# Kernel optimization log

Measured on AMD Instinct MI355X. Metric: run time of the kernel, lower is better.

The kernel has to match this reference:

```python
import jax, jax.numpy as jnp
import numpy as np

LORA_ALPHA = 16.0

def setup_inputs() -> dict:
    key = jax.random.key(0)
    kx, kw, ka, kb, kbias = jax.random.split(key, 5)
    B_, S, D_in, D_out, R = 2, 4096, 4096, 4096, 16
    x = jax.random.normal(kx, (B_, S, D_in), dtype=jnp.float32)
    W = jax.random.normal(kw, (D_out, D_in), dtype=jnp.float32) * 0.02
    A = jax.random.normal(ka, (R, D_in), dtype=jnp.float32) * 0.02
    Bm = jax.random.normal(kb, (D_out, R), dtype=jnp.float32) * 0.02
    bias = jax.random.normal(kbias, (D_out,), dtype=jnp.float32) * 0.02
    return {"x": x, "W": W, "A": A, "B": Bm, "bias": bias}

def reference(x, W, A, B, bias):
    # y = x @ W.T + bias + (alpha/rank) * (x @ A.T) @ B.T   (dropout p=0)
    rank = A.shape[0]
    lora_scale = LORA_ALPHA / rank
    y = jnp.einsum('bsd,nd->bsn', x, W) + bias
    h = jnp.einsum('bsd,rd->bsr', x, A)          # [B,S,r] low-rank down-proj
    y = y + lora_scale * jnp.einsum('bsr,nr->bsn', h, B)
    return y
```

## Files before the change

### kernel.cpp

```cpp
#include <hip/hip_runtime.h>
#include <hip/hip_bf16.h>

typedef short bf16x8 __attribute__((ext_vector_type(8)));
typedef float f32x4 __attribute__((ext_vector_type(4)));
typedef unsigned short ushort8v __attribute__((ext_vector_type(8)));

#define SBAR() asm volatile("s_barrier" ::: "memory")
#define LGKM0() do { asm volatile("s_waitcnt lgkmcnt(0)" ::: "memory"); \
    __builtin_amdgcn_sched_barrier(0); } while (0)

__device__ __forceinline__ unsigned short f2bf(float f) {
  unsigned u = __builtin_bit_cast(unsigned, f);
  u += 0x7fffu + ((u >> 16) & 1u);
  return (unsigned short)(u >> 16);
}

__device__ __forceinline__ void gload_lds16(const unsigned short* g, unsigned short* l) {
  __builtin_amdgcn_global_load_lds((const __attribute__((address_space(1))) void*)g,
                                   (__attribute__((address_space(3))) void*)l, 16, 0, 0);
}

__global__ __launch_bounds__(256) void prep_kernel(const float* __restrict__ x,
                                                   const float* __restrict__ W,
                                                   const float* __restrict__ A,
                                                   const float* __restrict__ Bm,
                                                   unsigned short* __restrict__ xb,
                                                   unsigned short* __restrict__ wb,
                                                   float scale, int K, int R, int n8, int t8) {
  int i = blockIdx.x * 256 + threadIdx.x;
  if (i < n8) {
    const float4* p = (const float4*)x + (size_t)i * 2;
    float4 a = p[0], b = p[1];
    ushort8v v;
    v[0] = f2bf(a.x); v[1] = f2bf(a.y); v[2] = f2bf(a.z); v[3] = f2bf(a.w);
    v[4] = f2bf(b.x); v[5] = f2bf(b.y); v[6] = f2bf(b.z); v[7] = f2bf(b.w);
    *((ushort8v*)xb + i) = v;
    return;
  }
  int idx = i - n8;
  if (idx >= t8) return;
  int perRow = K >> 3;
  int n = idx / perRow;
  int d0 = (idx - n * perRow) << 3;
  const float4* wp = (const float4*)(W + (size_t)n * K + d0);
  float4 w0 = wp[0], w1 = wp[1];
  float acc[8] = {w0.x, w0.y, w0.z, w0.w, w1.x, w1.y, w1.z, w1.w};
#pragma unroll 4
  for (int r = 0; r < R; ++r) {
    float c = Bm[(size_t)n * R + r] * scale;
    const float4* ap = (const float4*)(A + (size_t)r * K + d0);
    float4 a0 = ap[0], a1 = ap[1];
    acc[0] += c * a0.x; acc[1] += c * a0.y; acc[2] += c * a0.z; acc[3] += c * a0.w;
    acc[4] += c * a1.x; acc[5] += c * a1.y; acc[6] += c * a1.z; acc[7] += c * a1.w;
  }
  ushort8v v;
#pragma unroll
  for (int j = 0; j < 8; ++j) v[j] = f2bf(acc[j]);
  *((ushort8v*)wb + idx) = v;
}

__global__ __launch_bounds__(512, 2) void gemm256_bt_bias(const unsigned short* __restrict__ Xb,
                                                          const unsigned short* __restrict__ Wb,
                                                          const float* __restrict__ bias,
                                                          float* __restrict__ C,
                                                          int M, int N, int K) {
  __shared__ __align__(16) char lds[131072];
  const int t = threadIdx.x;
  const int wave = t >> 6, lane = t & 63;
  const int fr = lane & 15, kc = lane >> 4;
  const int wr = wave >> 2, wc = wave & 3;

  const int NTn = N >> 8;
  const int nwg = gridDim.x;
  int bid = blockIdx.x;
  if ((nwg & 7) == 0) bid = (bid & 7) * (nwg >> 3) + (bid >> 3);
  const int tm = bid / NTn, tn = bid % NTn;
  const int m0 = tm << 8, n0 = tn << 8;

  const int grow = t >> 3;
  const int gch8 = ((t & 7) ^ ((t >> 3) & 7)) << 3;
  const size_t K64 = (size_t)64 * K;
  const unsigned short* pa = Xb + (size_t)(m0 + grow) * K + gch8;
  const unsigned short* pb = Wb + (size_t)(n0 + grow) * K + gch8;
  char* const sb = (char*)lds + wave * 1024;

  const int sw  = (lane & 7) << 4;
  const int cb0 = (kc << 4) ^ sw;
  const int cb1 = cb0 ^ 64;
  const int rowA = (wr * 128 + fr) * 128;
  const int rowB = 32768 + (wc * 64 + fr) * 128;
  const char* rA0[2] = { (char*)lds + rowA + cb0, (char*)lds + 65536 + rowA + cb0 };
  const char* rA1[2] = { (char*)lds + rowA + cb1, (char*)lds + 65536 + rowA + cb1 };
  const char* rB0[2] = { (char*)lds + rowB + cb0, (char*)lds + 65536 + rowB + cb0 };
  const char* rB1[2] = { (char*)lds + rowB + cb1, (char*)lds + 65536 + rowB + cb1 };

  f32x4 acc[8][4];
#pragma unroll
  for (int m = 0; m < 8; ++m)
#pragma unroll
    for (int n = 0; n < 4; ++n) acc[m][n] = (f32x4){0.f, 0.f, 0.f, 0.f};

  bf16x8 aQa[8], aQb[8], bQ0[4], bQ1[4];
  const int NT = K >> 6;

#define STG_A1(BUF, s) gload_lds16(pa + (size_t)(s) * K64, \
    (unsigned short*)(sb + ((BUF) ? 65536 : 0) + (s) * 8192))
#define STG_B1(BUF, s) gload_lds16(pb + (size_t)(s) * K64, \
    (unsigned short*)(sb + ((BUF) ? 65536 : 0) + 32768 + (s) * 8192))

#define MM(qm, qn, AR, BR) do { \
    __builtin_amdgcn_s_setprio(1); \
    _Pragma("unroll") for (int ks = 0; ks < 2; ++ks) \
    _Pragma("unroll") for (int m = 0; m < 4; ++m) \
    _Pragma("unroll") for (int n = 0; n < 2; ++n) \
      acc[(qm)*4+m][(qn)*2+n] = __builtin_amdgcn_mfma_f32_16x16x32_bf16( \
          AR[m*2+ks], BR[n*2+ks], acc[(qm)*4+m][(qn)*2+n], 0, 0, 0); \
    __builtin_amdgcn_s_setprio(0); } while (0)

#define STEP(BUF, DOSTG, VM2, VM4) do { \
     \
    aQa[0]=*(const bf16x8*)(rA0[BUF]);        aQa[1]=*(const bf16x8*)(rA1[BUF]); \
    aQa[2]=*(const bf16x8*)(rA0[BUF]+2048);   aQa[3]=*(const bf16x8*)(rA1[BUF]+2048); \
    aQa[4]=*(const bf16x8*)(rA0[BUF]+4096);   aQa[5]=*(const bf16x8*)(rA1[BUF]+4096); \
    aQa[6]=*(const bf16x8*)(rA0[BUF]+6144);   aQa[7]=*(const bf16x8*)(rA1[BUF]+6144); \
    bQ0[0]=*(const bf16x8*)(rB0[BUF]);        bQ0[1]=*(const bf16x8*)(rB1[BUF]); \
    bQ0[2]=*(const bf16x8*)(rB0[BUF]+2048);   bQ0[3]=*(const bf16x8*)(rB1[BUF]+2048); \
    if (DOSTG) { STG_B1(BUF^1, 0); STG_B1(BUF^1, 1); } \
    asm volatile("s_waitcnt lgkmcnt(8)" ::: "memory"); \
    SBAR(); LGKM0(); MM(0, 0, aQa, bQ0); SBAR(); \
     \
    bQ1[0]=*(const bf16x8*)(rB0[BUF]+4096);   bQ1[1]=*(const bf16x8*)(rB1[BUF]+4096); \
    bQ1[2]=*(const bf16x8*)(rB0[BUF]+6144);   bQ1[3]=*(const bf16x8*)(rB1[BUF]+6144); \
    if (DOSTG) { STG_B1(BUF^1, 2); STG_B1(BUF^1, 3); } \
    asm volatile("s_waitcnt vmcnt(" VM2 ")" ::: "memory"); \
    SBAR(); LGKM0(); MM(0, 1, aQa, bQ1); SBAR(); \
     \
    aQb[0]=*(const bf16x8*)(rA0[BUF]+8192);   aQb[1]=*(const bf16x8*)(rA1[BUF]+8192); \
    aQb[2]=*(const bf16x8*)(rA0[BUF]+10240);  aQb[3]=*(const bf16x8*)(rA1[BUF]+10240); \
    aQb[4]=*(const bf16x8*)(rA0[BUF]+12288);  aQb[5]=*(const bf16x8*)(rA1[BUF]+12288); \
    aQb[6]=*(const bf16x8*)(rA0[BUF]+14336);  aQb[7]=*(const bf16x8*)(rA1[BUF]+14336); \
    if (DOSTG) { STG_A1(BUF^1, 0); STG_A1(BUF^1, 2); } \
    SBAR(); LGKM0(); MM(1, 0, aQb, bQ0); SBAR(); \
     \
    if (DOSTG) { STG_A1(BUF^1, 1); STG_A1(BUF^1, 3); pa += 64; pb += 64; } \
    asm volatile("s_waitcnt vmcnt(" VM4 ")" ::: "memory"); \
    SBAR(); MM(1, 1, aQb, bQ1); SBAR(); \
  } while (0)

  STG_B1(0, 0); STG_B1(0, 1); STG_B1(0, 2); STG_B1(0, 3);
  STG_A1(0, 0); STG_A1(0, 2); STG_A1(0, 1); STG_A1(0, 3);
  pa += 64; pb += 64;
  asm volatile("s_waitcnt vmcnt(2)" ::: "memory");
  SBAR();

  for (int cc = 0; cc < NT - 2; cc += 2) {
    STEP(0, 1, "4", "2");
    STEP(1, 1, "4", "2");
  }
  STEP(0, 1, "4", "2");
  STEP(1, 0, "0", "0");

  const int crow = (lane >> 4) * 4;
  const int ccol = lane & 15;
#pragma unroll
  for (int n = 0; n < 4; ++n) {
    int col = n0 + wc * 64 + n * 16 + ccol;
    float bv = bias[col];
#pragma unroll
    for (int m = 0; m < 8; ++m) {
      int row = m0 + wr * 128 + m * 16 + crow;
      float* cp = C + (size_t)row * N + col;
#pragma unroll
      for (int r = 0; r < 4; ++r) cp[(size_t)r * N] = acc[m][n][r] + bv;
    }
  }
#undef STG_A1
#undef STG_B1
#undef MM
#undef STEP
}

__global__ __launch_bounds__(256) void gemm_bt_bias(const unsigned short* __restrict__ Xb,
                                                    const unsigned short* __restrict__ Wb,
                                                    const float* __restrict__ bias,
                                                    float* __restrict__ C,
                                                    int M, int N, int K) {
  __shared__ unsigned short sA[128 * 32];
  __shared__ unsigned short sB[128 * 32];
  const int t = threadIdx.x;
  const int wave = t >> 6, lane = t & 63;
  const int NT = N >> 7;
  const int nwg = gridDim.x;
  int bid = blockIdx.x;
  if ((nwg & 7) == 0) bid = (bid & 7) * (nwg >> 3) + (bid >> 3);
  const int tm = bid / NT, tn = bid % NT;
  const int m0 = tm << 7, n0 = tn << 7;
  const int wr = wave >> 1, wc = wave & 1;

  f32x4 acc[4][4];
#pragma unroll
  for (int m = 0; m < 4; ++m)
#pragma unroll
    for (int n = 0; n < 4; ++n) acc[m][n] = (f32x4){0.f, 0.f, 0.f, 0.f};

  const unsigned short* gA0 = Xb + (size_t)(m0 + (t >> 2)) * K + (t & 3) * 8;
  const unsigned short* gA1 = Xb + (size_t)(m0 + 64 + (t >> 2)) * K + (t & 3) * 8;
  const unsigned short* gB0 = Wb + (size_t)(n0 + (t >> 2)) * K + (t & 3) * 8;
  const unsigned short* gB1 = Wb + (size_t)(n0 + 64 + (t >> 2)) * K + (t & 3) * 8;
  unsigned short* lA0 = sA + (size_t)(wave * 64) * 8;
  unsigned short* lA1 = sA + (size_t)(256 + wave * 64) * 8;
  unsigned short* lB0 = sB + (size_t)(wave * 64) * 8;
  unsigned short* lB1 = sB + (size_t)(256 + wave * 64) * 8;

  const int rrow = lane & 15;
  const int rk = (lane >> 4) * 8;

  for (int k0 = 0; k0 < K; k0 += 32) {
    gload_lds16(gA0 + k0, lA0);
    gload_lds16(gA1 + k0, lA1);
    gload_lds16(gB0 + k0, lB0);
    gload_lds16(gB1 + k0, lB1);
    __syncthreads();
    bf16x8 af[4], bfr[4];
#pragma unroll
    for (int m = 0; m < 4; ++m)
      af[m] = *(const bf16x8*)&sA[(size_t)(wr * 64 + m * 16 + rrow) * 32 + rk];
#pragma unroll
    for (int n = 0; n < 4; ++n)
      bfr[n] = *(const bf16x8*)&sB[(size_t)(wc * 64 + n * 16 + rrow) * 32 + rk];
#pragma unroll
    for (int m = 0; m < 4; ++m)
#pragma unroll
      for (int n = 0; n < 4; ++n)
        acc[m][n] = __builtin_amdgcn_mfma_f32_16x16x32_bf16(af[m], bfr[n], acc[m][n], 0, 0, 0);
    __syncthreads();
  }
  const int crow0 = (lane >> 4) * 4;
  const int ccol = lane & 15;
#pragma unroll
  for (int n = 0; n < 4; ++n) {
    int col = n0 + wc * 64 + n * 16 + ccol;
    float bv = bias[col];
#pragma unroll
    for (int m = 0; m < 4; ++m) {
      int row = m0 + wr * 64 + m * 16 + crow0;
      float* cp = C + (size_t)row * N + col;
#pragma unroll
      for (int r = 0; r < 4; ++r) cp[(size_t)r * N] = acc[m][n][r] + bv;
    }
  }
}

__global__ __launch_bounds__(64) void lora_h_kernel(const float* __restrict__ x,
                                                    const float* __restrict__ A,
                                                    float* __restrict__ h,
                                                    float scale, int K, int R) {
  int m = blockIdx.x, lane = threadIdx.x;
  float acc[16];
#pragma unroll
  for (int r = 0; r < 16; ++r) acc[r] = 0.f;
  for (int d = lane; d < K; d += 64) {
    float xv = x[(size_t)m * K + d];
    for (int r = 0; r < R; ++r) acc[r] += xv * A[(size_t)r * K + d];
  }
  for (int off = 32; off; off >>= 1)
    for (int r = 0; r < R; ++r) acc[r] += __shfl_down(acc[r], off);
  if (lane == 0)
    for (int r = 0; r < R; ++r) h[(size_t)m * R + r] = acc[r] * scale;
}

__global__ __launch_bounds__(256) void fgemm_fallback(const float* __restrict__ X,
                                                      const float* __restrict__ W,
                                                      const float* __restrict__ Bm,
                                                      const float* __restrict__ bias,
                                                      const float* __restrict__ h,
                                                      float* __restrict__ C,
                                                      int M, int N, int K, int R) {
  __shared__ float sX[64][20];
  __shared__ float sW[64][20];
  int nt = N >> 6;
  int bx = blockIdx.x % nt, by = blockIdx.x / nt;
  int m0 = by << 6, n0 = bx << 6;
  int t = threadIdx.x;
  int tx = t & 15, ty = t >> 4;
  float acc[4][4] = {};
  int lr = t >> 2, lc = (t & 3) << 2;
  for (int k0 = 0; k0 < K; k0 += 16) {
    *(float4*)&sX[lr][lc] = *(const float4*)&X[(size_t)(m0 + lr) * K + k0 + lc];
    *(float4*)&sW[lr][lc] = *(const float4*)&W[(size_t)(n0 + lr) * K + k0 + lc];
    __syncthreads();
#pragma unroll
    for (int kk = 0; kk < 16; ++kk) {
      float a[4], b[4];
#pragma unroll
      for (int i = 0; i < 4; ++i) a[i] = sX[ty * 4 + i][kk];
#pragma unroll
      for (int j = 0; j < 4; ++j) b[j] = sW[tx * 4 + j][kk];
#pragma unroll
      for (int i = 0; i < 4; ++i)
#pragma unroll
        for (int j = 0; j < 4; ++j) acc[i][j] += a[i] * b[j];
    }
    __syncthreads();
  }
#pragma unroll
  for (int i = 0; i < 4; ++i) {
    int row = m0 + ty * 4 + i;
#pragma unroll
    for (int j = 0; j < 4; ++j) {
      int col = n0 + tx * 4 + j;
      float lo = 0.f;
      for (int r = 0; r < R; ++r) lo += h[(size_t)row * R + r] * Bm[(size_t)col * R + r];
      C[(size_t)row * N + col] = acc[i][j] + bias[col] + lo;
    }
  }
}

extern "C" void kernel_launch(void* const* d_in, const int* in_sizes, int n_in,
                              void* d_out, int out_size, void* d_ws, size_t ws_size,
                              hipStream_t stream) {
  const float* x    = (const float*)d_in[0];
  const float* W    = (const float*)d_in[1];
  const float* A    = (const float*)d_in[2];
  const float* Bm   = (const float*)d_in[3];
  const float* bias = (const float*)d_in[4];
  float* out = (float*)d_out;

  const int N = in_sizes[4];
  const int R = in_sizes[3] / N;
  const int K = in_sizes[2] / R;
  const int M = in_sizes[0] / K;
  const float scale = 16.0f / (float)R;

  const size_t xbytes = (size_t)M * K * 2;
  const size_t wbytes = (size_t)N * K * 2;
  const bool ws_ok = (ws_size >= xbytes + wbytes);
  const bool fast256 = ws_ok && (M % 256 == 0) && (N % 256 == 0) && (K % 128 == 0) && (K >= 256);
  const bool fast128 = ws_ok && (M % 128 == 0) && (N % 128 == 0) && (K % 32 == 0);

  if (fast256 || fast128) {
    unsigned short* xb = (unsigned short*)d_ws;
    unsigned short* wb = (unsigned short*)((char*)d_ws + xbytes);
    int n8 = M * K / 8;
    int t8 = N * K / 8;
    int total = n8 + t8;
    prep_kernel<<<dim3((total + 255) / 256), dim3(256), 0, stream>>>(x, W, A, Bm, xb, wb,
                                                                     scale, K, R, n8, t8);
    if (fast256) {
      int grid = (M / 256) * (N / 256);
      gemm256_bt_bias<<<dim3(grid), dim3(512), 0, stream>>>(xb, wb, bias, out, M, N, K);
    } else {
      int grid = (M / 128) * (N / 128);
      gemm_bt_bias<<<dim3(grid), dim3(256), 0, stream>>>(xb, wb, bias, out, M, N, K);
    }
  } else {
    float* h = (float*)d_ws;
    lora_h_kernel<<<dim3(M), dim3(64), 0, stream>>>(x, A, h, scale, K, R);
    int grid = (M / 64) * (N / 64);
    fgemm_fallback<<<dim3(grid), dim3(256), 0, stream>>>(x, W, Bm, bias, h, out, M, N, K, R);
  }
}
```

Baseline: 338.4 us.

## Restructure 256x256 GEMM mainloop into triple-buffered A and double-buffered B pipeline

```diff
diff --git a/kernel.cpp b/kernel.cpp
--- a/kernel.cpp
+++ b/kernel.cpp
@@ -6,8 +6,6 @@
 typedef unsigned short ushort8v __attribute__((ext_vector_type(8)));
 
 #define SBAR() asm volatile("s_barrier" ::: "memory")
-#define LGKM0() do { asm volatile("s_waitcnt lgkmcnt(0)" ::: "memory"); \
-    __builtin_amdgcn_sched_barrier(0); } while (0)
 
 __device__ __forceinline__ unsigned short f2bf(float f) {
   unsigned u = __builtin_bit_cast(unsigned, f);
@@ -64,7 +62,7 @@
                                                           const float* __restrict__ bias,
                                                           float* __restrict__ C,
                                                           int M, int N, int K) {
-  __shared__ __align__(16) char lds[131072];
+  __shared__ __align__(16) char lds[163840];
   const int t = threadIdx.x;
   const int wave = t >> 6, lane = t & 63;
   const int fr = lane & 15, kc = lane >> 4;
@@ -82,17 +80,21 @@
   const size_t K64 = (size_t)64 * K;
   const unsigned short* pa = Xb + (size_t)(m0 + grow) * K + gch8;
   const unsigned short* pb = Wb + (size_t)(n0 + grow) * K + gch8;
-  char* const sb = (char*)lds + wave * 1024;
+  const int sdst = t * 16;
 
   const int sw  = (lane & 7) << 4;
   const int cb0 = (kc << 4) ^ sw;
   const int cb1 = cb0 ^ 64;
-  const int rowA = (wr * 128 + fr) * 128;
-  const int rowB = 32768 + (wc * 64 + fr) * 128;
-  const char* rA0[2] = { (char*)lds + rowA + cb0, (char*)lds + 65536 + rowA + cb0 };
-  const char* rA1[2] = { (char*)lds + rowA + cb1, (char*)lds + 65536 + rowA + cb1 };
-  const char* rB0[2] = { (char*)lds + rowB + cb0, (char*)lds + 65536 + rowB + cb0 };
-  const char* rB1[2] = { (char*)lds + rowB + cb1, (char*)lds + 65536 + rowB + cb1 };
+  const int arA0 = (wr * 128 + fr) * 128 + cb0;
+  const int arA1 = (wr * 128 + fr) * 128 + cb1;
+  const int arB0 = (wc * 64 + fr) * 128 + cb0;
+  const int arB1 = (wc * 64 + fr) * 128 + cb1;
+
+#define AB0 0
+#define AB1 32768
+#define AB2 65536
+#define BB0 98304
+#define BB1 131072
 
   f32x4 acc[8][4];
 #pragma unroll
@@ -100,65 +102,92 @@
 #pragma unroll
     for (int n = 0; n < 4; ++n) acc[m][n] = (f32x4){0.f, 0.f, 0.f, 0.f};
 
-  bf16x8 aQa[8], aQb[8], bQ0[4], bQ1[4];
+  bf16x8 aA[8], aB[8], bA[4], bB[4];
   const int NT = K >> 6;
 
-#define STG_A1(BUF, s) gload_lds16(pa + (size_t)(s) * K64, \
-    (unsigned short*)(sb + ((BUF) ? 65536 : 0) + (s) * 8192))
-#define STG_B1(BUF, s) gload_lds16(pb + (size_t)(s) * K64, \
-    (unsigned short*)(sb + ((BUF) ? 65536 : 0) + 32768 + (s) * 8192))
-
-#define MM(qm, qn, AR, BR) do { \
-    __builtin_amdgcn_s_setprio(1); \
+#define RD16(BI, LR) (*(const bf16x8*)((const char*)lds + (size_t)(BI) + (LR)))
+#define STGA(AS, s) gload_lds16(pa + (size_t)(s) * K64, \
+    (unsigned short*)((char*)lds + (AS) + (s) * 8192 + sdst))
+#define STGB(BS, s) gload_lds16(pb + (size_t)(s) * K64, \
+    (unsigned short*)((char*)lds + (BS) + (s) * 8192 + sdst))
+
+#define MMQ(MO, NO, AF, BF) do { \
     _Pragma("unroll") for (int ks = 0; ks < 2; ++ks) \
     _Pragma("unroll") for (int m = 0; m < 4; ++m) \
     _Pragma("unroll") for (int n = 0; n < 2; ++n) \
-      acc[(qm)*4+m][(qn)*2+n] = __builtin_amdgcn_mfma_f32_16x16x32_bf16( \
-          AR[m*2+ks], BR[n*2+ks], acc[(qm)*4+m][(qn)*2+n], 0, 0, 0); \
-    __builtin_amdgcn_s_setprio(0); } while (0)
-
-#define STEP(BUF, DOSTG, VM2, VM4) do { \
-     \
-    aQa[0]=*(const bf16x8*)(rA0[BUF]);        aQa[1]=*(const bf16x8*)(rA1[BUF]); \
-    aQa[2]=*(const bf16x8*)(rA0[BUF]+2048);   aQa[3]=*(const bf16x8*)(rA1[BUF]+2048); \
-    aQa[4]=*(const bf16x8*)(rA0[BUF]+4096);   aQa[5]=*(const bf16x8*)(rA1[BUF]+4096); \
-    aQa[6]=*(const bf16x8*)(rA0[BUF]+6144);   aQa[7]=*(const bf16x8*)(rA1[BUF]+6144); \
-    bQ0[0]=*(const bf16x8*)(rB0[BUF]);        bQ0[1]=*(const bf16x8*)(rB1[BUF]); \
-    bQ0[2]=*(const bf16x8*)(rB0[BUF]+2048);   bQ0[3]=*(const bf16x8*)(rB1[BUF]+2048); \
-    if (DOSTG) { STG_B1(BUF^1, 0); STG_B1(BUF^1, 1); } \
-    asm volatile("s_waitcnt lgkmcnt(8)" ::: "memory"); \
-    SBAR(); LGKM0(); MM(0, 0, aQa, bQ0); SBAR(); \
-     \
-    bQ1[0]=*(const bf16x8*)(rB0[BUF]+4096);   bQ1[1]=*(const bf16x8*)(rB1[BUF]+4096); \
-    bQ1[2]=*(const bf16x8*)(rB0[BUF]+6144);   bQ1[3]=*(const bf16x8*)(rB1[BUF]+6144); \
-    if (DOSTG) { STG_B1(BUF^1, 2); STG_B1(BUF^1, 3); } \
-    asm volatile("s_waitcnt vmcnt(" VM2 ")" ::: "memory"); \
-    SBAR(); LGKM0(); MM(0, 1, aQa, bQ1); SBAR(); \
-     \
-    aQb[0]=*(const bf16x8*)(rA0[BUF]+8192);   aQb[1]=*(const bf16x8*)(rA1[BUF]+8192); \
-    aQb[2]=*(const bf16x8*)(rA0[BUF]+10240);  aQb[3]=*(const bf16x8*)(rA1[BUF]+10240); \
-    aQb[4]=*(const bf16x8*)(rA0[BUF]+12288);  aQb[5]=*(const bf16x8*)(rA1[BUF]+12288); \
-    aQb[6]=*(const bf16x8*)(rA0[BUF]+14336);  aQb[7]=*(const bf16x8*)(rA1[BUF]+14336); \
-    if (DOSTG) { STG_A1(BUF^1, 0); STG_A1(BUF^1, 2); } \
-    SBAR(); LGKM0(); MM(1, 0, aQb, bQ0); SBAR(); \
-     \
-    if (DOSTG) { STG_A1(BUF^1, 1); STG_A1(BUF^1, 3); pa += 64; pb += 64; } \
-    asm volatile("s_waitcnt vmcnt(" VM4 ")" ::: "memory"); \
-    SBAR(); MM(1, 1, aQb, bQ1); SBAR(); \
-  } while (0)
-
-  STG_B1(0, 0); STG_B1(0, 1); STG_B1(0, 2); STG_B1(0, 3);
-  STG_A1(0, 0); STG_A1(0, 2); STG_A1(0, 1); STG_A1(0, 3);
+      acc[(MO)+m][(NO)+n] = __builtin_amdgcn_mfma_f32_16x16x32_bf16( \
+          AF[m*2+ks], BF[n*2+ks], acc[(MO)+m][(NO)+n], 0, 0, 0); } while (0)
+
+#define STEP(AR, BR, AN, BN, AS, BS, DOSTG, DOEARLY, VM1, VM2, LGM2) do { \
+   \
+  bB[0]=RD16((BR)+4096, arB0);     bB[1]=RD16((BR)+4096, arB1); \
+  bB[2]=RD16((BR)+6144, arB0);     bB[3]=RD16((BR)+6144, arB1); \
+  aB[0]=RD16((AR)+8192, arA0);     aB[1]=RD16((AR)+8192, arA1); \
+  if (DOSTG) { STGA(AS, 0); STGA(AS, 1); } \
+  SBAR(); \
+  asm volatile("s_waitcnt lgkmcnt(6)" ::: "memory"); __builtin_amdgcn_sched_barrier(0); \
+  __builtin_amdgcn_s_setprio(1); MMQ(0, 0, aA, bA); __builtin_amdgcn_s_setprio(0); \
+  SBAR(); \
+   \
+  aB[2]=RD16((AR)+10240, arA0);    aB[3]=RD16((AR)+10240, arA1); \
+  aB[4]=RD16((AR)+12288, arA0);    aB[5]=RD16((AR)+12288, arA1); \
+  aB[6]=RD16((AR)+14336, arA0);    aB[7]=RD16((AR)+14336, arA1); \
+  if (DOSTG) { STGA(AS, 2); STGA(AS, 3); } \
+  SBAR(); \
+  asm volatile("s_waitcnt lgkmcnt(8)" ::: "memory"); __builtin_amdgcn_sched_barrier(0); \
+  __builtin_amdgcn_s_setprio(1); MMQ(0, 2, aA, bB); __builtin_amdgcn_s_setprio(0); \
+  asm volatile("s_waitcnt vmcnt(" VM1 ")" ::: "memory"); \
+  SBAR(); \
+   \
+  if (DOEARLY) { \
+    aA[0]=RD16((AN), arA0);        aA[1]=RD16((AN), arA1); \
+    aA[2]=RD16((AN)+2048, arA0);   aA[3]=RD16((AN)+2048, arA1); \
+    aA[4]=RD16((AN)+4096, arA0);   aA[5]=RD16((AN)+4096, arA1); } \
+  if (DOSTG) { STGB(BS, 0); STGB(BS, 1); } \
+  SBAR(); \
+  asm volatile("s_waitcnt lgkmcnt(" LGM2 ")" ::: "memory"); __builtin_amdgcn_sched_barrier(0); \
+  __builtin_amdgcn_s_setprio(1); MMQ(4, 0, aB, bA); __builtin_amdgcn_s_setprio(0); \
+  asm volatile("s_waitcnt vmcnt(" VM2 ")" ::: "memory"); \
+  SBAR(); \
+   \
+  if (DOEARLY) { \
+    aA[6]=RD16((AN)+6144, arA0);   aA[7]=RD16((AN)+6144, arA1); \
+    bA[0]=RD16((BN), arB0);        bA[1]=RD16((BN), arB1); \
+    bA[2]=RD16((BN)+2048, arB0);   bA[3]=RD16((BN)+2048, arB1); } \
+  if (DOSTG) { STGB(BS, 2); STGB(BS, 3); pa += 64; pb += 64; } \
+  SBAR(); __builtin_amdgcn_sched_barrier(0); \
+  __builtin_amdgcn_s_setprio(1); MMQ(4, 2, aB, bB); __builtin_amdgcn_s_setprio(0); \
+  SBAR(); \
+} while (0)
+
+  STGA(AB0, 0); STGA(AB0, 1); STGA(AB0, 2); STGA(AB0, 3);
+  STGB(BB0, 0); STGB(BB0, 1); STGB(BB0, 2); STGB(BB0, 3);
   pa += 64; pb += 64;
-  asm volatile("s_waitcnt vmcnt(2)" ::: "memory");
+  STGA(AB1, 0); STGA(AB1, 1); STGA(AB1, 2); STGA(AB1, 3);
+  STGB(BB1, 0); STGB(BB1, 1); STGB(BB1, 2); STGB(BB1, 3);
+  pa += 64; pb += 64;
+  asm volatile("s_waitcnt vmcnt(8)" ::: "memory");
   SBAR();
-
-  for (int cc = 0; cc < NT - 2; cc += 2) {
-    STEP(0, 1, "4", "2");
-    STEP(1, 1, "4", "2");
-  }
-  STEP(0, 1, "4", "2");
-  STEP(1, 0, "0", "0");
+  aA[0]=RD16(AB0, arA0);      aA[1]=RD16(AB0, arA1);
+  aA[2]=RD16(AB0+2048, arA0); aA[3]=RD16(AB0+2048, arA1);
+  aA[4]=RD16(AB0+4096, arA0); aA[5]=RD16(AB0+4096, arA1);
+  aA[6]=RD16(AB0+6144, arA0); aA[7]=RD16(AB0+6144, arA1);
+  bA[0]=RD16(BB0, arB0);      bA[1]=RD16(BB0, arB1);
+  bA[2]=RD16(BB0+2048, arB0); bA[3]=RD16(BB0+2048, arB1);
+
+  const int packs = (NT - 4) / 6;
+  for (int it = 0; it < packs; ++it) {
+    STEP(AB0, BB0, AB1, BB1, AB2, BB0, 1, 1, "8", "6", "6");
+    STEP(AB1, BB1, AB2, BB0, AB0, BB1, 1, 1, "8", "6", "6");
+    STEP(AB2, BB0, AB0, BB1, AB1, BB0, 1, 1, "8", "6", "6");
+    STEP(AB0, BB1, AB1, BB0, AB2, BB1, 1, 1, "8", "6", "6");
+    STEP(AB1, BB0, AB2, BB1, AB0, BB0, 1, 1, "8", "6", "6");
+    STEP(AB2, BB1, AB0, BB0, AB1, BB1, 1, 1, "8", "6", "6");
+  }
+  STEP(AB0, BB0, AB1, BB1, AB2, BB0, 1, 1, "8", "6", "6");
+  STEP(AB1, BB1, AB2, BB0, AB0, BB1, 1, 1, "8", "6", "6");
+  STEP(AB2, BB0, AB0, BB1, AB1, BB0, 0, 1, "4", "0", "6");
+  STEP(AB0, BB1, AB1, BB0, AB2, BB1, 0, 0, "0", "0", "0");
 
   const int crow = (lane >> 4) * 4;
   const int ccol = lane & 15;
@@ -174,10 +203,16 @@
       for (int r = 0; r < 4; ++r) cp[(size_t)r * N] = acc[m][n][r] + bv;
     }
   }
-#undef STG_A1
-#undef STG_B1
-#undef MM
+#undef RD16
+#undef STGA
+#undef STGB
+#undef MMQ
 #undef STEP
+#undef AB0
+#undef AB1
+#undef AB2
+#undef BB0
+#undef BB1
 }
 
 __global__ __launch_bounds__(256) void gemm_bt_bias(const unsigned short* __restrict__ Xb,
@@ -335,7 +370,9 @@
   const size_t xbytes = (size_t)M * K * 2;
   const size_t wbytes = (size_t)N * K * 2;
   const bool ws_ok = (ws_size >= xbytes + wbytes);
-  const bool fast256 = ws_ok && (M % 256 == 0) && (N % 256 == 0) && (K % 128 == 0) && (K >= 256);
+  const int NT = K >> 6;
+  const bool fast256 = ws_ok && (M % 256 == 0) && (N % 256 == 0) && (K % 64 == 0) &&
+                       (NT % 6 == 4) && (NT >= 10);
   const bool fast128 = ws_ok && (M % 128 == 0) && (N % 128 == 0) && (K % 32 == 0);
 
   if (fast256 || fast128) {
```

New measurement: 827.0 us. 144% more time.
